# Performance work log

Measured on AMD Instinct MI355X. Metric: run time of the kernel, lower is better.

Reference implementation:

```python
import jax, jax.numpy as jnp
import numpy as np

B, S, D, H, KH, DH, L, V, MULT = 1, 2048, 2048, 16, 2, 128, 4, 10000, 4
INNER = D * MULT
EPS = 1e-5


def layernorm(x, g, b):
    m = jnp.mean(x, axis=-1, keepdims=True)
    v = jnp.var(x, axis=-1, keepdims=True)
    return (x - m) * jax.lax.rsqrt(v + EPS) * g + b


def setup_inputs() -> dict:
    key = jax.random.key(0)
    ks = jax.random.split(key, 24)
    s = lambda *shape: 0.02
    inp = {
        'text': jax.random.randint(ks[0], (B, S), 0, V),
        'embed_w': jax.random.normal(ks[1], (V, D), jnp.float32) * 0.02,
        # model-level LayerNorm (applied after embed and after every block)
        'model_norm_g': jnp.ones((D,), jnp.float32),
        'model_norm_b': jnp.zeros((D,), jnp.float32),
        # per-block params, stacked on leading L axis
        'blk_norm_g': jnp.ones((L, D), jnp.float32),
        'blk_norm_b': jnp.zeros((L, D), jnp.float32),
        'attn_norm_g': jnp.ones((L, D), jnp.float32),  # RingAttention prenorm
        'attn_norm_b': jnp.zeros((L, D), jnp.float32),
        'wq': jax.random.normal(ks[2], (L, D, H * DH), jnp.float32) * 0.02,
        'wk': jax.random.normal(ks[3], (L, D, KH * DH), jnp.float32) * 0.02,
        'wv': jax.random.normal(ks[4], (L, D, KH * DH), jnp.float32) * 0.02,
        'wo': jax.random.normal(ks[5], (L, H * DH, D), jnp.float32) * 0.02,
        'qn_g': jnp.ones((L, DH), jnp.float32),  # qk_norm LayerNorm scales
        'kn_g': jnp.ones((L, DH), jnp.float32),
        'w1': jax.random.normal(ks[6], (L, D, INNER), jnp.float32) * 0.02,
        'b1': jnp.zeros((L, INNER), jnp.float32),
        'w2': jax.random.normal(ks[7], (L, INNER, D), jnp.float32) * 0.02,
        'b2': jnp.zeros((L, D), jnp.float32),
        # output head: LayerNorm + Linear(D, V)
        'head_norm_g': jnp.ones((D,), jnp.float32),
        'head_norm_b': jnp.zeros((D,), jnp.float32),
        'head_w': jax.random.normal(ks[8], (D, V), jnp.float32) * 0.02,
        'head_b': jnp.zeros((V,), jnp.float32),
    }
    return inp


def _attention(xn, wq, wk, wv, wo, qn_g, kn_g):
    # xn: [B,S,D] (already prenormed)
    q = (xn @ wq).reshape(B, S, H, DH)
    k = (xn @ wk).reshape(B, S, KH, DH)
    v = (xn @ wv).reshape(B, S, KH, DH)
    # qk-norm: LayerNorm over head dim with learnable scale
    q = layernorm(q, qn_g, 0.0)
    k = layernorm(k, kn_g, 0.0)
    # GQA: expand kv heads to query heads
    rep = H // KH
    k = jnp.repeat(k, rep, axis=2)  # [B,S,H,DH]
    v = jnp.repeat(v, rep, axis=2)
    scale = DH ** -0.5
    scores = jnp.einsum('bqhd,bkhd->bhqk', q, k) * scale  # [B,H,S,S]
    causal = jnp.tril(jnp.ones((S, S), bool))
    scores = jnp.where(causal, scores, jnp.finfo(scores.dtype).min)
    p = jax.nn.softmax(scores, axis=-1)
    out = jnp.einsum('bhqk,bkhd->bqhd', p, v).reshape(B, S, H * DH)
    return out @ wo


def reference(text, embed_w, model_norm_g, model_norm_b, blk_norm_g, blk_norm_b,
              attn_norm_g, attn_norm_b, wq, wk, wv, wo, qn_g, kn_g,
              w1, b1, w2, b2, head_norm_g, head_norm_b, head_w, head_b):
    x = embed_w[text]                                # [B,S,D]
    x = layernorm(x, model_norm_g, model_norm_b)
    for i in range(L):
        h = layernorm(x, blk_norm_g[i], blk_norm_b[i])       # block norm
        hn = layernorm(h, attn_norm_g[i], attn_norm_b[i])    # attn prenorm
        h = _attention(hn, wq[i], wk[i], wv[i], wo[i], qn_g[i], kn_g[i]) + h
        ff = jax.nn.gelu(h @ w1[i] + b1[i]) @ w2[i] + b2[i]
        x = ff + h
        x = layernorm(x, model_norm_g, model_norm_b)
    x = layernorm(x, head_norm_g, head_norm_b)
    return x @ head_w + head_b                       # [B,S,V] logits
```

## Files before the change

kernel.cpp:

```cpp
#include <hip/hip_runtime.h>
#include <math.h>

#define S_LEN 2048
#define DMODEL 2048
#define NHEAD 16
#define KVHEAD 2
#define DHEAD 128
#define NLAYER 4
#define VOCAB 10000
#define INNER_DIM 8192
#define LN_EPS 1e-5f
#define VOCAB_PAD 10240
#define QKVN 2560

typedef __attribute__((ext_vector_type(4))) float f32x4;
typedef __attribute__((ext_vector_type(2))) float f32x2;
typedef __attribute__((ext_vector_type(8))) short s16x8;
typedef __attribute__((ext_vector_type(4))) short s16x4;

__device__ __forceinline__ short f2bf(float f) {
  union { float f; unsigned u; } v; v.f = f;
  unsigned r = v.u + 0x7FFFu + ((v.u >> 16) & 1u);
  return (short)(r >> 16);
}

__device__ __forceinline__ float gelu_tanh(float x) {
  float z = 0.7978845608028654f * (x + 0.044715f * x * x * x);
  float t = __expf(-2.0f * fabsf(z));
  float th = (1.0f - t) / (1.0f + t);
  th = copysignf(th, z);
  return 0.5f * x * (1.0f + th);
}

__device__ __forceinline__ void glds16(const void* g, void* l) {
  __builtin_amdgcn_global_load_lds(
      (const __attribute__((address_space(1))) unsigned int*)g,
      (__attribute__((address_space(3))) unsigned int*)l, 16, 0, 0);
}

__global__ __launch_bounds__(256)
void wtrans_all(const float* __restrict__ wq, const float* __restrict__ wk,
                const float* __restrict__ wv, const float* __restrict__ wo,
                const float* __restrict__ w1, const float* __restrict__ w2,
                short* __restrict__ wqkvT, short* __restrict__ woT,
                short* __restrict__ w1T, short* __restrict__ w2T) {
  __shared__ float ld[64][65];
  int b = blockIdx.x;
  const float* W; short* WT; int gx, K;
  if (b < 1024)      { W = wq; WT = wqkvT; gx = 32; K = 2048; }
  else if (b < 1152) { b -= 1024; W = wk; WT = wqkvT + (size_t)2048 * 2048; gx = 4; K = 2048; }
  else if (b < 1280) { b -= 1152; W = wv; WT = wqkvT + (size_t)2304 * 2048; gx = 4; K = 2048; }
  else if (b < 2304) { b -= 1280; W = wo; WT = woT; gx = 32; K = 2048; }
  else if (b < 6400) { b -= 2304; W = w1; WT = w1T; gx = 128; K = 2048; }
  else               { b -= 6400; W = w2; WT = w2T; gx = 32; K = 8192; }
  const int N = gx * 64;
  const int n0 = (b % gx) * 64, k0 = (b / gx) * 64;
  const int tid = threadIdx.x;
  const int rbase = tid >> 4;
  const int c4 = (tid & 15) * 4;
#pragma unroll
  for (int q = 0; q < 4; ++q) {
    int kk = rbase + q * 16;
    f32x4 v = *(const f32x4*)(W + (size_t)(k0 + kk) * N + n0 + c4);
    ld[kk][c4 + 0] = v[0]; ld[kk][c4 + 1] = v[1];
    ld[kk][c4 + 2] = v[2]; ld[kk][c4 + 3] = v[3];
  }
  __syncthreads();
#pragma unroll
  for (int s = 0; s < 2; ++s) {
    int lin = tid + s * 256;
    int nn = lin >> 3;
    int ks = lin & 7;
    s16x8 o;
#pragma unroll
    for (int j = 0; j < 8; ++j) o[j] = f2bf(ld[ks * 8 + j][nn]);
    *(s16x8*)&WT[(size_t)(n0 + nn) * K + k0 + ks * 8] = o;
  }
}

__global__ __launch_bounds__(256)
void wtrans64(const float* __restrict__ W, short* __restrict__ WT,
              int K, int N, int NP) {
  __shared__ float ld[64][65];
  const int n0 = blockIdx.x * 64, k0 = blockIdx.y * 64;
  const int tid = threadIdx.x;
  const int rbase = tid >> 4;
  const int c4 = (tid & 15) * 4;
#pragma unroll
  for (int q = 0; q < 4; ++q) {
    int kk = rbase + q * 16;
    const float* wp = W + (size_t)(k0 + kk) * N + n0 + c4;
    float v0, v1, v2, v3;
    if (n0 + c4 + 3 < N) {
      f32x4 v = *(const f32x4*)wp;
      v0 = v[0]; v1 = v[1]; v2 = v[2]; v3 = v[3];
    } else {
      v0 = (n0 + c4 + 0 < N) ? wp[0] : 0.f;
      v1 = (n0 + c4 + 1 < N) ? wp[1] : 0.f;
      v2 = (n0 + c4 + 2 < N) ? wp[2] : 0.f;
      v3 = (n0 + c4 + 3 < N) ? wp[3] : 0.f;
    }
    ld[kk][c4 + 0] = v0; ld[kk][c4 + 1] = v1;
    ld[kk][c4 + 2] = v2; ld[kk][c4 + 3] = v3;
  }
  __syncthreads();
#pragma unroll
  for (int s = 0; s < 2; ++s) {
    int lin = tid + s * 256;
    int nn = lin >> 3;
    int ks = lin & 7;
    int n = n0 + nn;
    if (n < NP) {
      s16x8 o;
#pragma unroll
      for (int j = 0; j < 8; ++j)
        o[j] = (n < N) ? f2bf(ld[ks * 8 + j][nn]) : (short)0;
      *(s16x8*)&WT[(size_t)n * K + k0 + ks * 8] = o;
    }
  }
}

__device__ __forceinline__ void ln3_core(
    float (&v)[8], int tid, int wave,
    const float* __restrict__ mg, const float* __restrict__ mb,
    const float* __restrict__ bg, const float* __restrict__ bb,
    const float* __restrict__ ag, const float* __restrict__ ab,
    float* __restrict__ hbrow, short* __restrict__ hnrow,
    float rs[3][4], float rs2[3][4]) {
#pragma unroll
  for (int rnd = 0; rnd < 3; ++rnd) {
    float s = 0.f, s2 = 0.f;
#pragma unroll
    for (int i = 0; i < 8; ++i) { s += v[i]; s2 += v[i] * v[i]; }
#pragma unroll
    for (int off = 1; off < 64; off <<= 1) {
      s += __shfl_xor(s, off); s2 += __shfl_xor(s2, off);
    }
    if ((tid & 63) == 0) { rs[rnd][wave] = s; rs2[rnd][wave] = s2; }
    __syncthreads();
    s = rs[rnd][0] + rs[rnd][1] + rs[rnd][2] + rs[rnd][3];
    s2 = rs2[rnd][0] + rs2[rnd][1] + rs2[rnd][2] + rs2[rnd][3];
    const float mean = s * (1.f / DMODEL);
    const float var = s2 * (1.f / DMODEL) - mean * mean;
    const float rstd = rsqrtf(var + LN_EPS);
    const float* gg = (rnd == 0) ? mg : (rnd == 1) ? bg : ag;
    const float* bbv = (rnd == 0) ? mb : (rnd == 1) ? bb : ab;
#pragma unroll
    for (int i = 0; i < 8; ++i) {
      int idx = tid + i * 256;
      v[i] = (v[i] - mean) * rstd * gg[idx] + bbv[idx];
    }
    if (rnd == 1) {
#pragma unroll
      for (int i = 0; i < 8; ++i) hbrow[tid + i * 256] = v[i];
    }
  }
#pragma unroll
  for (int i = 0; i < 8; ++i) hnrow[tid + i * 256] = f2bf(v[i]);
}

__global__ __launch_bounds__(256)
void ln_triple(const float* __restrict__ in,
               const float* __restrict__ mg, const float* __restrict__ mb,
               const float* __restrict__ bg, const float* __restrict__ bb,
               const float* __restrict__ ag, const float* __restrict__ ab,
               float* __restrict__ hb, short* __restrict__ hn16) {
  const int row = blockIdx.x;
  const int tid = threadIdx.x;
  const int wave = tid >> 6;
  __shared__ float rs[3][4], rs2[3][4];
  float v[8];
  const float* x = in + (size_t)row * DMODEL;
#pragma unroll
  for (int i = 0; i < 8; ++i) v[i] = x[tid + i * 256];
  ln3_core(v, tid, wave, mg, mb, bg, bb, ag, ab,
           hb + (size_t)row * DMODEL, hn16 + (size_t)row * DMODEL, rs, rs2);
}

__global__ __launch_bounds__(256)
void embed_ln3(const int* __restrict__ text, const float* __restrict__ ew,
               const float* __restrict__ mg, const float* __restrict__ mb,
               const float* __restrict__ bg, const float* __restrict__ bb,
               const float* __restrict__ ag, const float* __restrict__ ab,
               float* __restrict__ hb, short* __restrict__ hn16) {
  const int row = blockIdx.x;
  const int tid = threadIdx.x;
  const int wave = tid >> 6;
  __shared__ float rs[3][4], rs2[3][4];
  float v[8];
  const float* x = ew + (size_t)text[row] * DMODEL;
#pragma unroll
  for (int i = 0; i < 8; ++i) v[i] = x[tid + i * 256];
  ln3_core(v, tid, wave, mg, mb, bg, bb, ag, ab,
           hb + (size_t)row * DMODEL, hn16 + (size_t)row * DMODEL, rs, rs2);
}

__global__ __launch_bounds__(256)
void ln_dual(const float* __restrict__ in,
             const float* __restrict__ mg, const float* __restrict__ mb,
             const float* __restrict__ hg, const float* __restrict__ hbv,
             short* __restrict__ out16) {
  const int row = blockIdx.x;
  const int tid = threadIdx.x;
  const int wave = tid >> 6;
  __shared__ float rs[2][4], rs2[2][4];
  float v[8];
  const float* x = in + (size_t)row * DMODEL;
#pragma unroll
  for (int i = 0; i < 8; ++i) v[i] = x[tid + i * 256];
#pragma unroll
  for (int rnd = 0; rnd < 2; ++rnd) {
    float s = 0.f, s2 = 0.f;
#pragma unroll
    for (int i = 0; i < 8; ++i) { s += v[i]; s2 += v[i] * v[i]; }
#pragma unroll
    for (int off = 1; off < 64; off <<= 1) {
      s += __shfl_xor(s, off); s2 += __shfl_xor(s2, off);
    }
    if ((tid & 63) == 0) { rs[rnd][wave] = s; rs2[rnd][wave] = s2; }
    __syncthreads();
    s = rs[rnd][0] + rs[rnd][1] + rs[rnd][2] + rs[rnd][3];
    s2 = rs2[rnd][0] + rs2[rnd][1] + rs2[rnd][2] + rs2[rnd][3];
    const float mean = s * (1.f / DMODEL);
    const float var = s2 * (1.f / DMODEL) - mean * mean;
    const float rstd = rsqrtf(var + LN_EPS);
    const float* gg = (rnd == 0) ? mg : hg;
    const float* bbv = (rnd == 0) ? mb : hbv;
#pragma unroll
    for (int i = 0; i < 8; ++i) {
      int idx = tid + i * 256;
      v[i] = (v[i] - mean) * rstd * gg[idx] + bbv[idx];
    }
  }
  short* o = out16 + (size_t)row * DMODEL;
#pragma unroll
  for (int i = 0; i < 8; ++i) o[tid + i * 256] = f2bf(v[i]);
}

__global__ __launch_bounds__(256)
void vtrans_b16(const short* __restrict__ vb, short* __restrict__ vt) {
  __shared__ short ld[64][72];
  const int b = blockIdx.x;
  const int n0 = (b & 3) * 64, k0 = (b >> 2) * 64;
  const int tid = threadIdx.x;
  {
    int row = tid >> 2, s0 = (tid & 3) * 16;
    s16x8 a = *(const s16x8*)(vb + (size_t)(k0 + row) * 256 + n0 + s0);
    s16x8 c = *(const s16x8*)(vb + (size_t)(k0 + row) * 256 + n0 + s0 + 8);
    *(s16x8*)&ld[row][s0] = a;
    *(s16x8*)&ld[row][s0 + 8] = c;
  }
  __syncthreads();
  {
    int d = tid >> 2, seg = tid & 3;
    s16x8 o0, o1;
#pragma unroll
    for (int i = 0; i < 8; ++i) o0[i] = ld[seg * 16 + i][d];
#pragma unroll
    for (int i = 0; i < 8; ++i) o1[i] = ld[seg * 16 + 8 + i][d];
    *(s16x8*)&vt[(size_t)(n0 + d) * S_LEN + k0 + seg * 16] = o0;
    *(s16x8*)&vt[(size_t)(n0 + d) * S_LEN + k0 + seg * 16 + 8] = o1;
  }
}

template<int BM, int BN, int BK, int WM, int WN, int ACT, bool BIAS, bool RES,
         bool WF, bool WB>
__global__ __launch_bounds__(WM * WN * 64)
void gemm_db(const short* __restrict__ A, const short* __restrict__ BT,
             const float* __restrict__ bias, const float* __restrict__ res,
             float* __restrict__ Cf, short* __restrict__ Cb,
             int M, int N, int K) {
  constexpr int THREADS = WM * WN * 64;
  constexpr int MR = BM / WM / 16;
  constexpr int NR = BN / WN / 16;
  constexpr int KH = BK / 32;
  constexpr int SLOTS = BK / 8;
  constexpr int SMASK = SLOTS - 1;
  constexpr int RSH = (SLOTS == 8) ? 0 : 1;
  constexpr int CSH = (SLOTS == 8) ? 3 : 2;
  constexpr int NI = (BM * BK) / (THREADS * 8);
  __shared__ short As[2][BM * BK];
  __shared__ short Bs[2][BN * BK];
  const int tid = threadIdx.x;
  const int wave = tid >> 6, lane = tid & 63;
  const int g = lane >> 4, r = lane & 15;
  const int wm = wave / WN, wn = wave % WN;

  const int GY = gridDim.y;
  int lin = blockIdx.x + blockIdx.y * gridDim.x;
  int nwg = gridDim.x * GY;
  int sw = ((nwg & 7) == 0) ? ((lin & 7) * (nwg >> 3) + (lin >> 3)) : lin;
  const int bm = (sw % GY) * BM;
  const int bn = (sw / GY) * BN;

  const short* gsrc[2 * NI];
  short* ldst[2][2 * NI];
#pragma unroll
  for (int i = 0; i < NI; ++i) {
    int c = i * THREADS + tid;
    int row = c >> CSH;
    int slot = c & SMASK;
    int col = ((slot ^ ((row >> RSH) & SMASK)) << 3);
    gsrc[i] = A + (size_t)(bm + row) * K + col;
    gsrc[NI + i] = BT + (size_t)(bn + row) * K + col;
    int base = (i * THREADS + (wave << 6)) << 3;
    ldst[0][i] = &As[0][base]; ldst[0][NI + i] = &Bs[0][base];
    ldst[1][i] = &As[1][base]; ldst[1][NI + i] = &Bs[1][base];
  }

  f32x4 acc[MR][NR] = {};
  const int NT = K / BK;

#pragma unroll
  for (int i = 0; i < 2 * NI; ++i) glds16(gsrc[i], ldst[0][i]);
  asm volatile("s_waitcnt vmcnt(0)" ::: "memory");
  __syncthreads();

  for (int t = 0; t < NT; ++t) {
    const int cur = t & 1;
    const short* as = As[cur];
    const short* bs = Bs[cur];
    s16x8 bfr[NR][KH], af[MR / 2][KH];
#pragma unroll
    for (int n = 0; n < NR; ++n) {
      int rr = wn * (NR * 16) + n * 16 + r;
#pragma unroll
      for (int kk = 0; kk < KH; ++kk) {
        int lg = kk * 4 + g;
        bfr[n][kk] = *(const s16x8*)&bs[rr * BK + ((lg ^ ((rr >> RSH) & SMASK)) << 3)];
      }
    }
#pragma unroll
    for (int mm = 0; mm < MR / 2; ++mm) {
      int rr = wm * (MR * 16) + mm * 16 + r;
#pragma unroll
      for (int kk = 0; kk < KH; ++kk) {
        int lg = kk * 4 + g;
        af[mm][kk] = *(const s16x8*)&as[rr * BK + ((lg ^ ((rr >> RSH) & SMASK)) << 3)];
      }
    }
    if (t + 1 < NT) {
#pragma unroll
      for (int i = 0; i < 2 * NI; ++i) glds16(gsrc[i] + (t + 1) * BK, ldst[cur ^ 1][i]);
    }
    asm volatile("s_waitcnt lgkmcnt(0)" ::: "memory");
    __builtin_amdgcn_sched_barrier(0);
    __builtin_amdgcn_s_setprio(1);
#pragma unroll
    for (int mm = 0; mm < MR / 2; ++mm)
#pragma unroll
      for (int n = 0; n < NR; ++n)
#pragma unroll
        for (int kk = 0; kk < KH; ++kk)
          acc[mm][n] = __builtin_amdgcn_mfma_f32_16x16x32_bf16(af[mm][kk], bfr[n][kk], acc[mm][n], 0, 0, 0);
    __builtin_amdgcn_s_setprio(0);
    __builtin_amdgcn_s_barrier();
#pragma unroll
    for (int mm = 0; mm < MR / 2; ++mm) {
      int rr = wm * (MR * 16) + (MR / 2 + mm) * 16 + r;
#pragma unroll
      for (int kk = 0; kk < KH; ++kk) {
        int lg = kk * 4 + g;
        af[mm][kk] = *(const s16x8*)&as[rr * BK + ((lg ^ ((rr >> RSH) & SMASK)) << 3)];
      }
    }
    asm volatile("s_waitcnt lgkmcnt(0)" ::: "memory");
    __builtin_amdgcn_sched_barrier(0);
    __builtin_amdgcn_s_setprio(1);
#pragma unroll
    for (int mm = 0; mm < MR / 2; ++mm)
#pragma unroll
      for (int n = 0; n < NR; ++n)
#pragma unroll
        for (int kk = 0; kk < KH; ++kk)
          acc[MR / 2 + mm][n] = __builtin_amdgcn_mfma_f32_16x16x32_bf16(af[mm][kk], bfr[n][kk], acc[MR / 2 + mm][n], 0, 0, 0);
    __builtin_amdgcn_s_setprio(0);
    __syncthreads();
  }

#pragma unroll
  for (int m = 0; m < MR; ++m) {
    int row = bm + wm * (MR * 16) + m * 16 + g * 4;
#pragma unroll
    for (int n = 0; n < NR; ++n) {
      int col = bn + wn * (NR * 16) + n * 16 + r;
      if (col < N) {
#pragma unroll
        for (int j = 0; j < 4; ++j) {
          float v = acc[m][n][j];
          if (BIAS) v += bias[col];
          if (ACT) v = gelu_tanh(v);
          if (RES) v += res[(size_t)(row + j) * N + col];
          if (WF) Cf[(size_t)(row + j) * N + col] = v;
          if (WB) Cb[(size_t)(row + j) * N + col] = f2bf(v);
        }
      }
    }
  }
}

__global__ __launch_bounds__(256)
void gemm_qkv(const short* __restrict__ A, const short* __restrict__ BT,
              const float* __restrict__ qg, const float* __restrict__ kg,
              short* __restrict__ qb, short* __restrict__ kb,
              short* __restrict__ vb, int M, int K) {
  __shared__ short As[2][128 * 64];
  __shared__ short Bs[2][128 * 64];
  __shared__ float rsm[2][128], rs2m[2][128];
  const int tid = threadIdx.x;
  const int wave = tid >> 6, lane = tid & 63;
  const int g = lane >> 4, r = lane & 15;
  const int wm = wave >> 1, wn = wave & 1;

  const int GY = gridDim.y;
  int lin = blockIdx.x + blockIdx.y * gridDim.x;
  int nwg = gridDim.x * GY;
  int sw = (lin & 7) * (nwg >> 3) + (lin >> 3);
  const int bm = (sw % GY) * 128;
  const int bn = (sw / GY) * 128;

  const short* gsrc[8];
  short* ldst[2][8];
#pragma unroll
  for (int i = 0; i < 4; ++i) {
    int c = i * 256 + tid;
    int row = c >> 3;
    int slot = c & 7;
    int col = ((slot ^ (row & 7)) << 3);
    gsrc[i] = A + (size_t)(bm + row) * K + col;
    gsrc[4 + i] = BT + (size_t)(bn + row) * K + col;
    int base = (i * 256 + (wave << 6)) << 3;
    ldst[0][i] = &As[0][base]; ldst[0][4 + i] = &Bs[0][base];
    ldst[1][i] = &As[1][base]; ldst[1][4 + i] = &Bs[1][base];
  }

  f32x4 acc[4][4] = {};
  const int NT = K >> 6;

#pragma unroll
  for (int i = 0; i < 8; ++i) glds16(gsrc[i], ldst[0][i]);
  asm volatile("s_waitcnt vmcnt(0)" ::: "memory");
  __syncthreads();

  for (int t = 0; t < NT; ++t) {
    const int cur = t & 1;
    const short* as = As[cur];
    const short* bs = Bs[cur];
    s16x8 bfr[4][2], af[2][2];
#pragma unroll
    for (int n = 0; n < 4; ++n) {
      int rr = wn * 64 + n * 16 + r;
#pragma unroll
      for (int kk = 0; kk < 2; ++kk) {
        int lg = kk * 4 + g;
        bfr[n][kk] = *(const s16x8*)&bs[rr * 64 + ((lg ^ (rr & 7)) << 3)];
      }
    }
#pragma unroll
    for (int mm = 0; mm < 2; ++mm) {
      int rr = wm * 64 + mm * 16 + r;
#pragma unroll
      for (int kk = 0; kk < 2; ++kk) {
        int lg = kk * 4 + g;
        af[mm][kk] = *(const s16x8*)&as[rr * 64 + ((lg ^ (rr & 7)) << 3)];
      }
    }
    if (t + 1 < NT) {
#pragma unroll
      for (int i = 0; i < 8; ++i) glds16(gsrc[i] + (t + 1) * 64, ldst[cur ^ 1][i]);
    }
    asm volatile("s_waitcnt lgkmcnt(0)" ::: "memory");
    __builtin_amdgcn_sched_barrier(0);
    __builtin_amdgcn_s_setprio(1);
#pragma unroll
    for (int mm = 0; mm < 2; ++mm)
#pragma unroll
      for (int n = 0; n < 4; ++n)
#pragma unroll
        for (int kk = 0; kk < 2; ++kk)
          acc[mm][n] = __builtin_amdgcn_mfma_f32_16x16x32_bf16(af[mm][kk], bfr[n][kk], acc[mm][n], 0, 0, 0);
    __builtin_amdgcn_s_setprio(0);
    __builtin_amdgcn_s_barrier();
#pragma unroll
    for (int mm = 0; mm < 2; ++mm) {
      int rr = wm * 64 + (2 + mm) * 16 + r;
#pragma unroll
      for (int kk = 0; kk < 2; ++kk) {
        int lg = kk * 4 + g;
        af[mm][kk] = *(const s16x8*)&as[rr * 64 + ((lg ^ (rr & 7)) << 3)];
      }
    }
    asm volatile("s_waitcnt lgkmcnt(0)" ::: "memory");
    __builtin_amdgcn_sched_barrier(0);
    __builtin_amdgcn_s_setprio(1);
#pragma unroll
    for (int mm = 0; mm < 2; ++mm)
#pragma unroll
      for (int n = 0; n < 4; ++n)
#pragma unroll
        for (int kk = 0; kk < 2; ++kk)
          acc[2 + mm][n] = __builtin_amdgcn_mfma_f32_16x16x32_bf16(af[mm][kk], bfr[n][kk], acc[2 + mm][n], 0, 0, 0);
    __builtin_amdgcn_s_setprio(0);
    __syncthreads();
  }

  if (bn >= 2304) {
#pragma unroll
    for (int m = 0; m < 4; ++m) {
      int row = bm + wm * 64 + m * 16 + g * 4;
#pragma unroll
      for (int n = 0; n < 4; ++n) {
        int cl = wn * 64 + n * 16 + r;
#pragma unroll
        for (int j = 0; j < 4; ++j)
          vb[(size_t)(row + j) * 256 + (bn - 2304) + cl] = f2bf(acc[m][n][j]);
      }
    }
  } else {
    float ms[4][4], m2[4][4];
#pragma unroll
    for (int m = 0; m < 4; ++m)
#pragma unroll
      for (int j = 0; j < 4; ++j) {
        float s = 0.f, s2 = 0.f;
#pragma unroll
        for (int n = 0; n < 4; ++n) { float v = acc[m][n][j]; s += v; s2 += v * v; }
#pragma unroll
        for (int off = 1; off < 16; off <<= 1) {
          s += __shfl_xor(s, off); s2 += __shfl_xor(s2, off);
        }
        ms[m][j] = s; m2[m][j] = s2;
      }
    if (r == 0) {
#pragma unroll
      for (int m = 0; m < 4; ++m)
#pragma unroll
        for (int j = 0; j < 4; ++j) {
          int rl = wm * 64 + m * 16 + g * 4 + j;
          rsm[wn][rl] = ms[m][j]; rs2m[wn][rl] = m2[m][j];
        }
    }
    __syncthreads();
    const float* gv = (bn < 2048) ? qg : kg;
#pragma unroll
    for (int m = 0; m < 4; ++m)
#pragma unroll
      for (int j = 0; j < 4; ++j) {
        int rl = wm * 64 + m * 16 + g * 4 + j;
        float s = rsm[0][rl] + rsm[1][rl];
        float s2 = rs2m[0][rl] + rs2m[1][rl];
        float mean = s * (1.f / 128.f);
        float var = s2 * (1.f / 128.f) - mean * mean;
        float rstd = rsqrtf(var + LN_EPS);
        int srow = bm + rl;
#pragma unroll
        for (int n = 0; n < 4; ++n) {
          int cl = wn * 64 + n * 16 + r;
          float v = (acc[m][n][j] - mean) * rstd * gv[cl];
          if (bn < 2048) qb[(size_t)srow * 2048 + bn + cl] = f2bf(v);
          else kb[(size_t)srow * 256 + (bn - 2048) + cl] = f2bf(v);
        }
      }
  }
}

template<int ACT, bool BIAS, bool WF, bool WB>
__global__ __launch_bounds__(512, 2)
void gemm_8ph(const short* __restrict__ A, const short* __restrict__ BT,
              const float* __restrict__ bias,
              float* __restrict__ Cf, short* __restrict__ Cb,
              int M, int N, int K) {
  __shared__ short As[2][2][128 * 64];
  __shared__ short Bs[2][2][128 * 64];
  const int tid = threadIdx.x;
  const int wave = tid >> 6, lane = tid & 63;
  const int g = lane >> 4, r = lane & 15;
  const int wm = wave >> 2, wn = wave & 3;

  const int GY = gridDim.y;
  int lin = blockIdx.x + blockIdx.y * gridDim.x;
  int nwg = gridDim.x * GY;
  int sw = (lin & 7) * (nwg >> 3) + (lin >> 3);
  const int bm = (sw % GY) * 256;
  const int bn = (sw / GY) * 256;

  int rl[2], csw[2], ldo[2];
#pragma unroll
  for (int i = 0; i < 2; ++i) {
    int c = i * 512 + tid;
    rl[i] = c >> 3;
    csw[i] = (((c & 7) ^ (rl[i] & 7)) << 3);
    ldo[i] = (i * 512 + (wave << 6)) << 3;
  }
  const int NT = K >> 6;

  auto stA = [&](int t, int h, int d) {
#pragma unroll
    for (int i = 0; i < 2; ++i)
      glds16(A + (size_t)(bm + h * 128 + rl[i]) * K + t * 64 + csw[i], &As[d][h][ldo[i]]);
  };
  auto stB = [&](int t, int h, int d) {
#pragma unroll
    for (int i = 0; i < 2; ++i)
      glds16(BT + (size_t)(bn + h * 128 + rl[i]) * K + t * 64 + csw[i], &Bs[d][h][ldo[i]]);
  };

  stA(0, 0, 0); stA(0, 1, 0); stB(0, 0, 0); stB(0, 1, 0);
  stA(1, 0, 1);
  asm volatile("s_waitcnt vmcnt(2)" ::: "memory");
  asm volatile("s_barrier" ::: "memory");

  f32x4 acc[8][4] = {};
  s16x8 af[4][2], bf0[2][2], bf1[2][2];
  const int brow = (wn & 1) * 64;
  const int U = NT >> 1;

  for (int u = 0; u < U; ++u) {
    const int t1 = 2 * u + 1;
    const int q0 = (2 * u + 2 < NT) ? 2 * u + 2 : 0;
    const int q1 = (2 * u + 3 < NT) ? 2 * u + 3 : 0;
#pragma unroll
    for (int d = 0; d < 2; ++d) {
      const short* as = As[d][wm];
      const short* bsl = Bs[d][wn >> 1];
#pragma unroll
      for (int m = 0; m < 4; ++m)
#pragma unroll
        for (int kk = 0; kk < 2; ++kk)
          af[m][kk] = *(const s16x8*)&as[(m * 16 + r) * 64 + (((kk * 4 + g) ^ (r & 7)) << 3)];
#pragma unroll
      for (int n = 0; n < 2; ++n)
#pragma unroll
        for (int kk = 0; kk < 2; ++kk)
          bf0[n][kk] = *(const s16x8*)&bsl[(brow + n * 16 + r) * 64 + (((kk * 4 + g) ^ (r & 7)) << 3)];
      if (d == 0) stA(t1, 1, 1); else stA(q0, 1, 0);
      asm volatile("s_waitcnt lgkmcnt(0)" ::: "memory");
      __builtin_amdgcn_sched_barrier(0);
      __builtin_amdgcn_s_setprio(1);
#pragma unroll
      for (int m = 0; m < 4; ++m)
#pragma unroll
        for (int n = 0; n < 2; ++n)
#pragma unroll
          for (int kk = 0; kk < 2; ++kk)
            acc[m][n] = __builtin_amdgcn_mfma_f32_16x16x32_bf16(af[m][kk], bf0[n][kk], acc[m][n], 0, 0, 0);
      __builtin_amdgcn_s_setprio(0);
      asm volatile("s_barrier" ::: "memory");
#pragma unroll
      for (int n = 0; n < 2; ++n)
#pragma unroll
        for (int kk = 0; kk < 2; ++kk)
          bf1[n][kk] = *(const s16x8*)&bsl[(brow + (n + 2) * 16 + r) * 64 + (((kk * 4 + g) ^ (r & 7)) << 3)];
      if (d == 0) stB(t1, 0, 1); else stB(q0, 0, 0);
      asm volatile("s_waitcnt lgkmcnt(0)" ::: "memory");
      __builtin_amdgcn_sched_barrier(0);
      __builtin_amdgcn_s_setprio(1);
#pragma unroll
      for (int m = 0; m < 4; ++m)
#pragma unroll
        for (int n = 0; n < 2; ++n)
#pragma unroll
          for (int kk = 0; kk < 2; ++kk)
            acc[m][n + 2] = __builtin_amdgcn_mfma_f32_16x16x32_bf16(af[m][kk], bf1[n][kk], acc[m][n + 2], 0, 0, 0);
      __builtin_amdgcn_s_setprio(0);
      asm volatile("s_barrier" ::: "memory");
#pragma unroll
      for (int m = 0; m < 4; ++m)
#pragma unroll
        for (int kk = 0; kk < 2; ++kk)
          af[m][kk] = *(const s16x8*)&as[((m + 4) * 16 + r) * 64 + (((kk * 4 + g) ^ (r & 7)) << 3)];
      if (d == 0) stB(t1, 1, 1); else stB(q0, 1, 0);
      asm volatile("s_waitcnt lgkmcnt(0)" ::: "memory");
      __builtin_amdgcn_sched_barrier(0);
      __builtin_amdgcn_s_setprio(1);
#pragma unroll
      for (int m = 0; m < 4; ++m)
#pragma unroll
        for (int n = 0; n < 2; ++n)
#pragma unroll
          for (int kk = 0; kk < 2; ++kk)
            acc[m + 4][n + 2] = __builtin_amdgcn_mfma_f32_16x16x32_bf16(af[m][kk], bf1[n][kk], acc[m + 4][n + 2], 0, 0, 0);
      __builtin_amdgcn_s_setprio(0);
      asm volatile("s_barrier" ::: "memory");
      if (d == 0) stA(q0, 0, 0); else stA(q1, 0, 1);
      __builtin_amdgcn_s_setprio(1);
#pragma unroll
      for (int m = 0; m < 4; ++m)
#pragma unroll
        for (int n = 0; n < 2; ++n)
#pragma unroll
          for (int kk = 0; kk < 2; ++kk)
            acc[m + 4][n] = __builtin_amdgcn_mfma_f32_16x16x32_bf16(af[m][kk], bf0[n][kk], acc[m + 4][n], 0, 0, 0);
      __builtin_amdgcn_s_setprio(0);
      asm volatile("s_waitcnt vmcnt(2)" ::: "memory");
      asm volatile("s_barrier" ::: "memory");
    }
  }
  asm volatile("s_waitcnt vmcnt(0)" ::: "memory");

#pragma unroll
  for (int m = 0; m < 8; ++m) {
    int row = bm + wm * 128 + m * 16 + g * 4;
#pragma unroll
    for (int n = 0; n < 4; ++n) {
      int col = bn + wn * 64 + n * 16 + r;
      if (col < N) {
#pragma unroll
        for (int j = 0; j < 4; ++j) {
          float v = acc[m][n][j];
          if (BIAS) v += bias[col];
          if (ACT) v = gelu_tanh(v);
          if (WF) Cf[(size_t)(row + j) * N + col] = v;
          if (WB) Cb[(size_t)(row + j) * N + col] = f2bf(v);
        }
      }
    }
  }
}

__global__ __launch_bounds__(256)
void attn_fwd3(const short* __restrict__ qbuf, const short* __restrict__ kbuf,
               const short* __restrict__ vtb, short* __restrict__ obuf) {
  __shared__ short Qs[64 * 128];
  __shared__ short Ks[64 * 128];
  __shared__ short Vt[128 * 64];
  __shared__ short Ps[4][16][88];
  const int tid = threadIdx.x;
  int lin = blockIdx.x + blockIdx.y * gridDim.x;
  int sw = (lin & 7) * 32 + (lin >> 3);
  const int pair = sw & 15;
  const int h = sw >> 4;
  const int kh = h >> 3;
  const int wave = tid >> 6, lane = tid & 63;
  const int g = lane >> 4, r = lane & 15;
  const float scale = 0.08838834764831845f;

#pragma unroll
  for (int half = 0; half < 2; ++half) {
    const int qt = half ? (31 - pair) : pair;
    const int qbase = qt * 64;
    __builtin_amdgcn_s_barrier();
#pragma unroll
    for (int i = 0; i < 4; ++i) {
      int c = i * 256 + tid;
      int row = c >> 4;
      int scol = (((c & 15) ^ (row & 7)) << 3);
      glds16(qbuf + (size_t)(qbase + row) * DMODEL + h * DHEAD + scol,
             &Qs[(i * 256 + (wave << 6)) << 3]);
    }
    f32x4 O[8] = {};
    float mst[4], lst[4];
#pragma unroll
    for (int j = 0; j < 4; ++j) { mst[j] = -1e30f; lst[j] = 0.f; }
    s16x8 aq[4];

    for (int jt = 0; jt <= qt; ++jt) {
      const int jb = jt * 64;
      if (jt) __builtin_amdgcn_s_barrier();
#pragma unroll
      for (int i = 0; i < 4; ++i) {
        int c = i * 256 + tid;
        int row = c >> 4;
        int scol = (((c & 15) ^ (row & 7)) << 3);
        glds16(kbuf + (size_t)(jb + row) * 256 + kh * DHEAD + scol,
               &Ks[(i * 256 + (wave << 6)) << 3]);
      }
#pragma unroll
      for (int i = 0; i < 4; ++i) {
        int c = i * 256 + tid;
        int row = c >> 3;
        int scol = (((c & 7) ^ (row & 7)) << 3);
        glds16(vtb + (size_t)(kh * 128 + row) * S_LEN + jb + scol,
               &Vt[(i * 256 + (wave << 6)) << 3]);
      }
      asm volatile("s_waitcnt vmcnt(4)" ::: "memory");
      __builtin_amdgcn_s_barrier();
      if (jt == 0) {
#pragma unroll
        for (int kc = 0; kc < 4; ++kc) {
          int rr = wave * 16 + r;
          aq[kc] = *(const s16x8*)&Qs[rr * 128 + ((((kc << 2) | g) ^ (rr & 7)) << 3)];
        }
      }
      f32x4 sc[4] = {};
      __builtin_amdgcn_s_setprio(1);
#pragma unroll
      for (int n = 0; n < 4; ++n) {
        int rr = n * 16 + r;
#pragma unroll
        for (int kc = 0; kc < 4; ++kc) {
          s16x8 bk = *(const s16x8*)&Ks[rr * 128 + ((((kc << 2) | g) ^ (rr & 7)) << 3)];
          sc[n] = __builtin_amdgcn_mfma_f32_16x16x32_bf16(aq[kc], bk, sc[n], 0, 0, 0);
        }
      }
      __builtin_amdgcn_s_setprio(0);
      if (jt == qt) {
#pragma unroll
        for (int j = 0; j < 4; ++j) {
          int irow = qbase + wave * 16 + g * 4 + j;
#pragma unroll
          for (int n = 0; n < 4; ++n) {
            int jcol = jb + n * 16 + r;
            sc[n][j] = (jcol <= irow) ? sc[n][j] * scale : -1e30f;
          }
        }
      } else {
#pragma unroll
        for (int j = 0; j < 4; ++j)
#pragma unroll
          for (int n = 0; n < 4; ++n) sc[n][j] *= scale;
      }
      float pmax[4], alpha[4], rsum[4];
#pragma unroll
      for (int j = 0; j < 4; ++j)
        pmax[j] = fmaxf(fmaxf(sc[0][j], sc[1][j]), fmaxf(sc[2][j], sc[3][j]));
#pragma unroll
      for (int off = 1; off < 16; off <<= 1)
#pragma unroll
        for (int j = 0; j < 4; ++j) pmax[j] = fmaxf(pmax[j], __shfl_xor(pmax[j], off));
#pragma unroll
      for (int j = 0; j < 4; ++j) {
        float mnew = fmaxf(mst[j], pmax[j]);
        alpha[j] = __expf(mst[j] - mnew);
        mst[j] = mnew;
#pragma unroll
        for (int n = 0; n < 4; ++n) sc[n][j] = __expf(sc[n][j] - mnew);
        rsum[j] = (sc[0][j] + sc[1][j]) + (sc[2][j] + sc[3][j]);
      }
#pragma unroll
      for (int off = 1; off < 16; off <<= 1)
#pragma unroll
        for (int j = 0; j < 4; ++j) rsum[j] += __shfl_xor(rsum[j], off);
#pragma unroll
      for (int j = 0; j < 4; ++j) lst[j] = lst[j] * alpha[j] + rsum[j];
#pragma unroll
      for (int d = 0; d < 8; ++d)
#pragma unroll
        for (int j = 0; j < 4; ++j) O[d][j] *= alpha[j];
      asm volatile("s_waitcnt vmcnt(0)" ::: "memory");
      __builtin_amdgcn_s_barrier();
#pragma unroll
      for (int j = 0; j < 4; ++j)
#pragma unroll
        for (int n = 0; n < 4; ++n)
          Ps[wave][g * 4 + j][n * 16 + r] = f2bf(sc[n][j]);
      s16x8 pa0 = *(const s16x8*)&Ps[wave][r][g * 8];
      s16x8 pa1 = *(const s16x8*)&Ps[wave][r][32 + g * 8];
      __builtin_amdgcn_s_setprio(1);
#pragma unroll
      for (int d = 0; d < 8; ++d) {
        int dd = d * 16 + r;
        s16x8 b0 = *(const s16x8*)&Vt[dd * 64 + ((g ^ (dd & 7)) << 3)];
        s16x8 b1 = *(const s16x8*)&Vt[dd * 64 + (((4 + g) ^ (dd & 7)) << 3)];
        O[d] = __builtin_amdgcn_mfma_f32_16x16x32_bf16(pa0, b0, O[d], 0, 0, 0);
        O[d] = __builtin_amdgcn_mfma_f32_16x16x32_bf16(pa1, b1, O[d], 0, 0, 0);
      }
      __builtin_amdgcn_s_setprio(0);
    }
    float linv[4];
#pragma unroll
    for (int j = 0; j < 4; ++j) linv[j] = 1.f / lst[j];
#pragma unroll
    for (int d = 0; d < 8; ++d)
#pragma unroll
      for (int j = 0; j < 4; ++j)
        obuf[(size_t)(qbase + wave * 16 + g * 4 + j) * DMODEL + h * DHEAD + d * 16 + r] =
            f2bf(O[d][j] * linv[j]);
  }
}

extern "C" void kernel_launch(void* const* d_in, const int* in_sizes, int n_in,
                              void* d_out, int out_size, void* d_ws, size_t ws_size,
                              hipStream_t stream) {
  const int* text = (const int*)d_in[0];
  const float* embed_w = (const float*)d_in[1];
  const float* model_g = (const float*)d_in[2];
  const float* model_b = (const float*)d_in[3];
  const float* blk_g = (const float*)d_in[4];
  const float* blk_b = (const float*)d_in[5];
  const float* attn_g = (const float*)d_in[6];
  const float* attn_b = (const float*)d_in[7];
  const float* wq = (const float*)d_in[8];
  const float* wk = (const float*)d_in[9];
  const float* wv = (const float*)d_in[10];
  const float* wo = (const float*)d_in[11];
  const float* qn_g = (const float*)d_in[12];
  const float* kn_g = (const float*)d_in[13];
  const float* w1 = (const float*)d_in[14];
  const float* b1 = (const float*)d_in[15];
  const float* w2 = (const float*)d_in[16];
  const float* b2 = (const float*)d_in[17];
  const float* head_g = (const float*)d_in[18];
  const float* head_b = (const float*)d_in[19];
  const float* head_w = (const float*)d_in[20];
  const float* head_bias = (const float*)d_in[21];
  float* out = (float*)d_out;

  const size_t SD = (size_t)S_LEN * DMODEL;
  const size_t SKV = (size_t)S_LEN * KVHEAD * DHEAD;
  const size_t SI = (size_t)S_LEN * INNER_DIM;
  const size_t WD = (size_t)DMODEL * DMODEL;
  const size_t WKV = (size_t)DMODEL * KVHEAD * DHEAD;
  const size_t WI = (size_t)DMODEL * INNER_DIM;

  char* p = (char*)d_ws;
  float* xres  = (float*)p; p += SD * 4;
  float* hb    = (float*)p; p += SD * 4;
  float* h2    = (float*)p; p += SD * 4;
  short* hn16  = (short*)p; p += SD * 2;
  short* h216  = (short*)p; p += SD * 2;
  short* ao16  = (short*)p; p += SD * 2;
  short* ffi16 = (short*)p; p += SI * 2;
  short* qb16  = (short*)p; p += SD * 2;
  short* kb16  = (short*)p; p += SKV * 2;
  short* vb16  = (short*)p; p += SKV * 2;
  short* vt16  = (short*)p; p += SKV * 2;
  short* wqkvT = (short*)p; p += (size_t)QKVN * DMODEL * 2;
  short* woT   = (short*)p; p += WD * 2;
  short* w1T   = (short*)p; p += WI * 2;
  short* w2T   = (short*)p; p += WI * 2;
  short* headT = w1T;

  dim3 blk(256);
  embed_ln3<<<S_LEN, blk, 0, stream>>>(text, embed_w, model_g, model_b,
                                       blk_g, blk_b, attn_g, attn_b, hb, hn16);

  for (int i = 0; i < NLAYER; ++i) {
    wtrans_all<<<10496, blk, 0, stream>>>(
        wq + (size_t)i * WD, wk + (size_t)i * WKV, wv + (size_t)i * WKV,
        wo + (size_t)i * WD, w1 + (size_t)i * WI, w2 + (size_t)i * WI,
        wqkvT, woT, w1T, w2T);

    gemm_qkv<<<dim3(QKVN / 128, S_LEN / 128), blk, 0, stream>>>(
        hn16, wqkvT, qn_g + i * DHEAD, kn_g + i * DHEAD,
        qb16, kb16, vb16, S_LEN, DMODEL);

    vtrans_b16<<<128, blk, 0, stream>>>(vb16, vt16);

    attn_fwd3<<<dim3(16, 16), blk, 0, stream>>>(qb16, kb16, vt16, ao16);

    gemm_db<128, 128, 64, 2, 2, 0, false, true, true, true>
        <<<dim3(DMODEL / 128, S_LEN / 128), blk, 0, stream>>>(
        ao16, woT, nullptr, hb, h2, h216, S_LEN, DMODEL, DMODEL);
    gemm_8ph<1, true, false, true>
        <<<dim3(INNER_DIM / 256, S_LEN / 256), dim3(512), 0, stream>>>(
        h216, w1T, b1 + (size_t)i * INNER_DIM, nullptr, ffi16, S_LEN, INNER_DIM, DMODEL);
    gemm_db<128, 128, 64, 2, 2, 0, true, true, true, false>
        <<<dim3(DMODEL / 128, S_LEN / 128), blk, 0, stream>>>(
        ffi16, w2T, b2 + (size_t)i * DMODEL, h2, xres, nullptr, S_LEN, DMODEL, INNER_DIM);

    if (i + 1 < NLAYER) {
      ln_triple<<<S_LEN, blk, 0, stream>>>(
          xres, model_g, model_b,
          blk_g + (i + 1) * DMODEL, blk_b + (i + 1) * DMODEL,
          attn_g + (i + 1) * DMODEL, attn_b + (i + 1) * DMODEL, hb, hn16);
    }
  }

  wtrans64<<<dim3(VOCAB_PAD / 64, 32), blk, 0, stream>>>(head_w, headT, DMODEL, VOCAB, VOCAB_PAD);
  ln_dual<<<S_LEN, blk, 0, stream>>>(xres, model_g, model_b, head_g, head_b, hn16);
  gemm_8ph<0, true, true, false>
      <<<dim3(VOCAB_PAD / 256, S_LEN / 256), dim3(512), 0, stream>>>(
      hn16, headT, head_bias, out, nullptr, S_LEN, VOCAB, DMODEL);
}
```

Baseline: 1.658 ms.

## Fuse V transpose into QKV GEMM epilogue and replace 8-phase GEMM with gemm_db

The QKV GEMM now transposes V tiles through shared memory in its epilogue and writes V^T directly, which removes the separate vtrans kernel and the intermediate V buffer. Separately, the hand-scheduled 8-phase 256x256 GEMM used for the FFN up-projection and the output head is deleted, and those calls now go to the generic double-buffered gemm_db template at 256x256 tiles with 8 waves. The fusion saves one launch and one round trip of V through memory. Swapping out the tuned 8-phase GEMM risks losing its interleaved load/MFMA scheduling and its occupancy hint on the two largest GEMMs.

```diff
diff --git a/kernel.cpp b/kernel.cpp
--- a/kernel.cpp
+++ b/kernel.cpp
@@ -235,32 +235,6 @@
   short* o = out16 + (size_t)row * DMODEL;
 #pragma unroll
   for (int i = 0; i < 8; ++i) o[tid + i * 256] = f2bf(v[i]);
-}
-
-__global__ __launch_bounds__(256)
-void vtrans_b16(const short* __restrict__ vb, short* __restrict__ vt) {
-  __shared__ short ld[64][72];
-  const int b = blockIdx.x;
-  const int n0 = (b & 3) * 64, k0 = (b >> 2) * 64;
-  const int tid = threadIdx.x;
-  {
-    int row = tid >> 2, s0 = (tid & 3) * 16;
-    s16x8 a = *(const s16x8*)(vb + (size_t)(k0 + row) * 256 + n0 + s0);
-    s16x8 c = *(const s16x8*)(vb + (size_t)(k0 + row) * 256 + n0 + s0 + 8);
-    *(s16x8*)&ld[row][s0] = a;
-    *(s16x8*)&ld[row][s0 + 8] = c;
-  }
-  __syncthreads();
-  {
-    int d = tid >> 2, seg = tid & 3;
-    s16x8 o0, o1;
-#pragma unroll
-    for (int i = 0; i < 8; ++i) o0[i] = ld[seg * 16 + i][d];
-#pragma unroll
-    for (int i = 0; i < 8; ++i) o1[i] = ld[seg * 16 + 8 + i][d];
-    *(s16x8*)&vt[(size_t)(n0 + d) * S_LEN + k0 + seg * 16] = o0;
-    *(s16x8*)&vt[(size_t)(n0 + d) * S_LEN + k0 + seg * 16 + 8] = o1;
-  }
 }
 
 template<int BM, int BN, int BK, int WM, int WN, int ACT, bool BIAS, bool RES,
@@ -403,7 +377,7 @@
 void gemm_qkv(const short* __restrict__ A, const short* __restrict__ BT,
               const float* __restrict__ qg, const float* __restrict__ kg,
               short* __restrict__ qb, short* __restrict__ kb,
-              short* __restrict__ vb, int M, int K) {
+              short* __restrict__ vt, int M, int K) {
   __shared__ short As[2][128 * 64];
   __shared__ short Bs[2][128 * 64];
   __shared__ float rsm[2][128], rs2m[2][128];
@@ -505,16 +479,28 @@
   }
 
   if (bn >= 2304) {
+    short* ld = &As[0][0];
 #pragma unroll
     for (int m = 0; m < 4; ++m) {
-      int row = bm + wm * 64 + m * 16 + g * 4;
+      int sl = wm * 64 + m * 16 + g * 4;
 #pragma unroll
       for (int n = 0; n < 4; ++n) {
-        int cl = wn * 64 + n * 16 + r;
+        int dl = wn * 64 + n * 16 + r;
 #pragma unroll
         for (int j = 0; j < 4; ++j)
-          vb[(size_t)(row + j) * 256 + (bn - 2304) + cl] = f2bf(acc[m][n][j]);
-      }
+          ld[(sl + j) * 128 + dl] = f2bf(acc[m][n][j]);
+      }
+    }
+    __syncthreads();
+    const int dl = tid & 127;
+    const int sh = (tid >> 7) * 64;
+    short* dst = vt + (size_t)(bn - 2304 + dl) * S_LEN + bm + sh;
+#pragma unroll
+    for (int v = 0; v < 8; ++v) {
+      s16x8 o;
+#pragma unroll
+      for (int i = 0; i < 8; ++i) o[i] = ld[(sh + v * 8 + i) * 128 + dl];
+      *(s16x8*)(dst + v * 8) = o;
     }
   } else {
     float ms[4][4], m2[4][4];
@@ -561,160 +547,6 @@
           else kb[(size_t)srow * 256 + (bn - 2048) + cl] = f2bf(v);
         }
       }
-  }
-}
-
-template<int ACT, bool BIAS, bool WF, bool WB>
-__global__ __launch_bounds__(512, 2)
-void gemm_8ph(const short* __restrict__ A, const short* __restrict__ BT,
-              const float* __restrict__ bias,
-              float* __restrict__ Cf, short* __restrict__ Cb,
-              int M, int N, int K) {
-  __shared__ short As[2][2][128 * 64];
-  __shared__ short Bs[2][2][128 * 64];
-  const int tid = threadIdx.x;
-  const int wave = tid >> 6, lane = tid & 63;
-  const int g = lane >> 4, r = lane & 15;
-  const int wm = wave >> 2, wn = wave & 3;
-
-  const int GY = gridDim.y;
-  int lin = blockIdx.x + blockIdx.y * gridDim.x;
-  int nwg = gridDim.x * GY;
-  int sw = (lin & 7) * (nwg >> 3) + (lin >> 3);
-  const int bm = (sw % GY) * 256;
-  const int bn = (sw / GY) * 256;
-
-  int rl[2], csw[2], ldo[2];
-#pragma unroll
-  for (int i = 0; i < 2; ++i) {
-    int c = i * 512 + tid;
-    rl[i] = c >> 3;
-    csw[i] = (((c & 7) ^ (rl[i] & 7)) << 3);
-    ldo[i] = (i * 512 + (wave << 6)) << 3;
-  }
-  const int NT = K >> 6;
-
-  auto stA = [&](int t, int h, int d) {
-#pragma unroll
-    for (int i = 0; i < 2; ++i)
-      glds16(A + (size_t)(bm + h * 128 + rl[i]) * K + t * 64 + csw[i], &As[d][h][ldo[i]]);
-  };
-  auto stB = [&](int t, int h, int d) {
-#pragma unroll
-    for (int i = 0; i < 2; ++i)
-      glds16(BT + (size_t)(bn + h * 128 + rl[i]) * K + t * 64 + csw[i], &Bs[d][h][ldo[i]]);
-  };
-
-  stA(0, 0, 0); stA(0, 1, 0); stB(0, 0, 0); stB(0, 1, 0);
-  stA(1, 0, 1);
-  asm volatile("s_waitcnt vmcnt(2)" ::: "memory");
-  asm volatile("s_barrier" ::: "memory");
-
-  f32x4 acc[8][4] = {};
-  s16x8 af[4][2], bf0[2][2], bf1[2][2];
-  const int brow = (wn & 1) * 64;
-  const int U = NT >> 1;
-
-  for (int u = 0; u < U; ++u) {
-    const int t1 = 2 * u + 1;
-    const int q0 = (2 * u + 2 < NT) ? 2 * u + 2 : 0;
-    const int q1 = (2 * u + 3 < NT) ? 2 * u + 3 : 0;
-#pragma unroll
-    for (int d = 0; d < 2; ++d) {
-      const short* as = As[d][wm];
-      const short* bsl = Bs[d][wn >> 1];
-#pragma unroll
-      for (int m = 0; m < 4; ++m)
-#pragma unroll
-        for (int kk = 0; kk < 2; ++kk)
-          af[m][kk] = *(const s16x8*)&as[(m * 16 + r) * 64 + (((kk * 4 + g) ^ (r & 7)) << 3)];
-#pragma unroll
-      for (int n = 0; n < 2; ++n)
-#pragma unroll
-        for (int kk = 0; kk < 2; ++kk)
-          bf0[n][kk] = *(const s16x8*)&bsl[(brow + n * 16 + r) * 64 + (((kk * 4 + g) ^ (r & 7)) << 3)];
-      if (d == 0) stA(t1, 1, 1); else stA(q0, 1, 0);
-      asm volatile("s_waitcnt lgkmcnt(0)" ::: "memory");
-      __builtin_amdgcn_sched_barrier(0);
-      __builtin_amdgcn_s_setprio(1);
-#pragma unroll
-      for (int m = 0; m < 4; ++m)
-#pragma unroll
-        for (int n = 0; n < 2; ++n)
-#pragma unroll
-          for (int kk = 0; kk < 2; ++kk)
-            acc[m][n] = __builtin_amdgcn_mfma_f32_16x16x32_bf16(af[m][kk], bf0[n][kk], acc[m][n], 0, 0, 0);
-      __builtin_amdgcn_s_setprio(0);
-      asm volatile("s_barrier" ::: "memory");
-#pragma unroll
-      for (int n = 0; n < 2; ++n)
-#pragma unroll
-        for (int kk = 0; kk < 2; ++kk)
-          bf1[n][kk] = *(const s16x8*)&bsl[(brow + (n + 2) * 16 + r) * 64 + (((kk * 4 + g) ^ (r & 7)) << 3)];
-      if (d == 0) stB(t1, 0, 1); else stB(q0, 0, 0);
-      asm volatile("s_waitcnt lgkmcnt(0)" ::: "memory");
-      __builtin_amdgcn_sched_barrier(0);
-      __builtin_amdgcn_s_setprio(1);
-#pragma unroll
-      for (int m = 0; m < 4; ++m)
-#pragma unroll
-        for (int n = 0; n < 2; ++n)
-#pragma unroll
-          for (int kk = 0; kk < 2; ++kk)
-            acc[m][n + 2] = __builtin_amdgcn_mfma_f32_16x16x32_bf16(af[m][kk], bf1[n][kk], acc[m][n + 2], 0, 0, 0);
-      __builtin_amdgcn_s_setprio(0);
-      asm volatile("s_barrier" ::: "memory");
-#pragma unroll
-      for (int m = 0; m < 4; ++m)
-#pragma unroll
-        for (int kk = 0; kk < 2; ++kk)
-          af[m][kk] = *(const s16x8*)&as[((m + 4) * 16 + r) * 64 + (((kk * 4 + g) ^ (r & 7)) << 3)];
-      if (d == 0) stB(t1, 1, 1); else stB(q0, 1, 0);
-      asm volatile("s_waitcnt lgkmcnt(0)" ::: "memory");
-      __builtin_amdgcn_sched_barrier(0);
-      __builtin_amdgcn_s_setprio(1);
-#pragma unroll
-      for (int m = 0; m < 4; ++m)
-#pragma unroll
-        for (int n = 0; n < 2; ++n)
-#pragma unroll
-          for (int kk = 0; kk < 2; ++kk)
-            acc[m + 4][n + 2] = __builtin_amdgcn_mfma_f32_16x16x32_bf16(af[m][kk], bf1[n][kk], acc[m + 4][n + 2], 0, 0, 0);
-      __builtin_amdgcn_s_setprio(0);
-      asm volatile("s_barrier" ::: "memory");
-      if (d == 0) stA(q0, 0, 0); else stA(q1, 0, 1);
-      __builtin_amdgcn_s_setprio(1);
-#pragma unroll
-      for (int m = 0; m < 4; ++m)
-#pragma unroll
-        for (int n = 0; n < 2; ++n)
-#pragma unroll
-          for (int kk = 0; kk < 2; ++kk)
-            acc[m + 4][n] = __builtin_amdgcn_mfma_f32_16x16x32_bf16(af[m][kk], bf0[n][kk], acc[m + 4][n], 0, 0, 0);
-      __builtin_amdgcn_s_setprio(0);
-      asm volatile("s_waitcnt vmcnt(2)" ::: "memory");
-      asm volatile("s_barrier" ::: "memory");
-    }
-  }
-  asm volatile("s_waitcnt vmcnt(0)" ::: "memory");
-
-#pragma unroll
-  for (int m = 0; m < 8; ++m) {
-    int row = bm + wm * 128 + m * 16 + g * 4;
-#pragma unroll
-    for (int n = 0; n < 4; ++n) {
-      int col = bn + wn * 64 + n * 16 + r;
-      if (col < N) {
-#pragma unroll
-        for (int j = 0; j < 4; ++j) {
-          float v = acc[m][n][j];
-          if (BIAS) v += bias[col];
-          if (ACT) v = gelu_tanh(v);
-          if (WF) Cf[(size_t)(row + j) * N + col] = v;
-          if (WB) Cb[(size_t)(row + j) * N + col] = f2bf(v);
-        }
-      }
-    }
   }
 }
 
@@ -913,7 +745,6 @@
   short* ffi16 = (short*)p; p += SI * 2;
   short* qb16  = (short*)p; p += SD * 2;
   short* kb16  = (short*)p; p += SKV * 2;
-  short* vb16  = (short*)p; p += SKV * 2;
   short* vt16  = (short*)p; p += SKV * 2;
   short* wqkvT = (short*)p; p += (size_t)QKVN * DMODEL * 2;
   short* woT   = (short*)p; p += WD * 2;
@@ -933,18 +764,17 @@
 
     gemm_qkv<<<dim3(QKVN / 128, S_LEN / 128), blk, 0, stream>>>(
         hn16, wqkvT, qn_g + i * DHEAD, kn_g + i * DHEAD,
-        qb16, kb16, vb16, S_LEN, DMODEL);
-
-    vtrans_b16<<<128, blk, 0, stream>>>(vb16, vt16);
+        qb16, kb16, vt16, S_LEN, DMODEL);
 
     attn_fwd3<<<dim3(16, 16), blk, 0, stream>>>(qb16, kb16, vt16, ao16);
 
     gemm_db<128, 128, 64, 2, 2, 0, false, true, true, true>
         <<<dim3(DMODEL / 128, S_LEN / 128), blk, 0, stream>>>(
         ao16, woT, nullptr, hb, h2, h216, S_LEN, DMODEL, DMODEL);
-    gemm_8ph<1, true, false, true>
+    gemm_db<256, 256, 64, 2, 4, 1, true, false, false, true>
         <<<dim3(INNER_DIM / 256, S_LEN / 256), dim3(512), 0, stream>>>(
-        h216, w1T, b1 + (size_t)i * INNER_DIM, nullptr, ffi16, S_LEN, INNER_DIM, DMODEL);
+        h216, w1T, b1 + (size_t)i * INNER_DIM, nullptr, nullptr, ffi16,
+        S_LEN, INNER_DIM, DMODEL);
     gemm_db<128, 128, 64, 2, 2, 0, true, true, true, false>
         <<<dim3(DMODEL / 128, S_LEN / 128), blk, 0, stream>>>(
         ffi16, w2T, b2 + (size_t)i * DMODEL, h2, xres, nullptr, S_LEN, DMODEL, INNER_DIM);
@@ -959,7 +789,7 @@
 
   wtrans64<<<dim3(VOCAB_PAD / 64, 32), blk, 0, stream>>>(head_w, headT, DMODEL, VOCAB, VOCAB_PAD);
   ln_dual<<<S_LEN, blk, 0, stream>>>(xres, model_g, model_b, head_g, head_b, hn16);
-  gemm_8ph<0, true, true, false>
+  gemm_db<256, 256, 64, 2, 4, 0, true, false, true, false>
       <<<dim3(VOCAB_PAD / 256, S_LEN / 256), dim3(512), 0, stream>>>(
-      hn16, headT, head_bias, out, nullptr, S_LEN, VOCAB, DMODEL);
-}
+      hn16, headT, head_bias, nullptr, out, nullptr, S_LEN, VOCAB, DMODEL);
+}
```

Measured after the change: 1.641 ms. About the same (-1.0%).
